# Kernel optimization log

Hardware: AMD Instinct MI355X
Metric: run time of the kernel (lower is better)

The kernel has to match this reference:

```python
import jax, jax.numpy as jnp
import numpy as np

D = 128  # input_dim

def setup_inputs() -> dict:
    key = jax.random.key(0)
    ks = jax.random.split(key, 9)
    B, Lq, Lkv = 4, 4096, 4096
    s = 1.0 / np.sqrt(D)
    return {
        "x1": jax.random.normal(ks[0], (B, Lq, D), dtype=jnp.float32),
        "x2": jax.random.normal(ks[1], (B, Lkv, D), dtype=jnp.float32),
        "x3": jax.random.normal(ks[2], (B, Lkv, D), dtype=jnp.float32),
        "Wq": jax.random.normal(ks[3], (D, D), dtype=jnp.float32) * s,
        "bq": jax.random.normal(ks[4], (D,), dtype=jnp.float32) * s,
        "Wk": jax.random.normal(ks[5], (D, D), dtype=jnp.float32) * s,
        "bk": jax.random.normal(ks[6], (D,), dtype=jnp.float32) * s,
        "Wv": jax.random.normal(ks[7], (D, D), dtype=jnp.float32) * s,
        "bv": jax.random.normal(ks[8], (D,), dtype=jnp.float32) * s,
    }

def reference(x1, x2, x3, Wq, bq, Wk, bk, Wv, bv):
    # torch Linear: y = x @ W.T + b
    q = jnp.einsum('bld,ed->ble', x1, Wq) + bq  # [B,Lq,D]
    k = jnp.einsum('bld,ed->ble', x2, Wk) + bk  # [B,Lkv,D]
    v = jnp.einsum('bld,ed->ble', x3, Wv) + bv  # [B,Lkv,D]
    scores = jnp.einsum('bqd,bkd->bqk', q, k) / jnp.sqrt(jnp.float32(x1.shape[-1]))
    attn = jax.nn.softmax(scores, axis=2)
    return jnp.einsum('bqk,bkd->bqd', attn, v)
```

## Files before the change

kernel.cpp:

```cpp
#include <hip/hip_runtime.h>
#include <hip/hip_bf16.h>

typedef __attribute__((ext_vector_type(8))) short short8;
typedef __attribute__((ext_vector_type(4))) float v4f;

__device__ __forceinline__ unsigned short f2bf(float f) {
    union { float f; unsigned u; } c; c.f = f;
    unsigned r = c.u + 0x7FFFu + ((c.u >> 16) & 1u);
    return (unsigned short)(r >> 16);
}
__device__ __forceinline__ unsigned pack2(float a, float b) {
    return (unsigned)f2bf(a) | ((unsigned)f2bf(b) << 16);
}
__device__ __forceinline__ float bf2f(unsigned short h) {
    union { unsigned u; float f; } c; c.u = ((unsigned)h) << 16;
    return c.f;
}

__device__ __forceinline__ void g2l16(const unsigned short* g, unsigned short* l) {
    __builtin_amdgcn_global_load_lds(
        (const __attribute__((address_space(1))) unsigned int*)g,
        (__attribute__((address_space(3))) unsigned int*)l,
        16, 0, 0);
}

__global__ __launch_bounds__(512) void proj_kernel(
    const float* __restrict__ x1, const float* __restrict__ x2, const float* __restrict__ x3,
    const float* __restrict__ Wq, const float* __restrict__ bq,
    const float* __restrict__ Wk, const float* __restrict__ bk,
    const float* __restrict__ Wv, const float* __restrict__ bv,
    unsigned short* __restrict__ qb, unsigned short* __restrict__ kb,
    unsigned short* __restrict__ vb, float qscale)
{
    __shared__ __attribute__((aligned(16))) unsigned short Xs[16384];
    __shared__ __attribute__((aligned(16))) unsigned short Ws[16384];

    int tid = threadIdx.x;
    int wave = tid >> 6, lane = tid & 63;
    int lmod = lane & 15, ldiv = lane >> 4;
    int p = blockIdx.x % 3;
    int row0 = (blockIdx.x / 3) * 128;

    const float* X = p == 0 ? x1 : p == 1 ? x2 : x3;
    const float* W = p == 0 ? Wq : p == 1 ? Wk : Wv;
    const float* bias = p == 0 ? bq : p == 1 ? bk : bv;
    float scale = p == 0 ? qscale : 1.0f;

#pragma unroll
    for (int i = 0; i < 8; i++) {
        int c = tid + i * 512;
        int row = c >> 5, d0 = (c & 31) * 4;
        v4f f = *(const v4f*)(X + (size_t)(row0 + row) * 128 + d0);
        int off = ((row >> 4) * 16 + (d0 >> 5) * 4 + ((d0 >> 3) & 3)) * 128 + (row & 15) * 8 + (d0 & 7);
        *(uint2*)&Xs[off] = make_uint2(pack2(f[0], f[1]), pack2(f[2], f[3]));
        v4f g = *(const v4f*)(W + (size_t)row * 128 + d0);
        *(uint2*)&Ws[off] = make_uint2(pack2(g[0], g[1]), pack2(g[2], g[3]));
    }
    __syncthreads();

    short8 af[4];
#pragma unroll
    for (int kc = 0; kc < 4; kc++)
        af[kc] = *(const short8*)&Xs[wave * 2048 + (kc * 4 + ldiv) * 128 + lmod * 8];

#pragma unroll
    for (int ct = 0; ct < 8; ct++) {
        v4f acc = {0.f, 0.f, 0.f, 0.f};
#pragma unroll
        for (int kc = 0; kc < 4; kc++) {
            short8 bf = *(const short8*)&Ws[ct * 2048 + (kc * 4 + ldiv) * 128 + lmod * 8];
            acc = __builtin_amdgcn_mfma_f32_16x16x32_bf16(af[kc], bf, acc, 0, 0, 0);
        }
        int e = ct * 16 + lmod;
        float bv_ = bias[e];
#pragma unroll
        for (int r = 0; r < 4; r++) {
            int orow = row0 + wave * 16 + ldiv * 4 + r;
            unsigned short h = f2bf((acc[r] + bv_) * scale);
            if (p == 0) {
                qb[(size_t)orow * 128 + e] = h;
            } else if (p == 1) {
                int b = orow >> 12, key = orow & 4095, kk = key & 31;
                kb[b * 524288 + (key >> 5) * 4096 + (kk & 1) * 2048
                   + ((e >> 5) * 4 + ((e >> 3) & 3)) * 128 + (kk >> 1) * 8 + (e & 7)] = h;
            } else {
                int b = orow >> 12, key = orow & 4095;
                vb[b * 524288 + (key >> 5) * 4096
                   + ((e >> 4) * 4 + ((key >> 3) & 3)) * 128 + (e & 15) * 8 + (key & 7)] = h;
            }
        }
    }
}

__global__ __launch_bounds__(256, 2) void attn_kernel(
    const unsigned short* __restrict__ Qb,
    const unsigned short* __restrict__ Kb,
    const unsigned short* __restrict__ Vb,
    unsigned short* __restrict__ Opart,
    float* __restrict__ Lbuf)
{
    __shared__ __attribute__((aligned(16))) unsigned short Kt[2][4096];
    __shared__ __attribute__((aligned(16))) unsigned short Vt[2][4096];
    __shared__ __attribute__((aligned(16))) unsigned short Ps[4][1280];

    int tid = threadIdx.x;
    int wave = tid >> 6, lane = tid & 63;
    int lmod = lane & 15, ldiv = lane >> 4;
    int split = blockIdx.x & 3;
    int qidx = blockIdx.x >> 2;
    int b = qidx >> 5;
    int q0 = (qidx & 31) * 128 + wave * 32;

    short8 qfrag[2][4];
#pragma unroll
    for (int set = 0; set < 2; set++) {
        const unsigned short* qptr = Qb + (size_t)(b * 4096 + q0 + set * 16 + lmod) * 128;
#pragma unroll
        for (int kc = 0; kc < 4; kc++)
            qfrag[set][kc] = *(const short8*)(qptr + kc * 32 + ldiv * 8);
    }

    v4f oacc[2][8];
#pragma unroll
    for (int set = 0; set < 2; set++)
#pragma unroll
        for (int dt = 0; dt < 8; dt++) oacc[set][dt] = (v4f){0.f, 0.f, 0.f, 0.f};
    float lsum[2][4] = {{0.f, 0.f, 0.f, 0.f}, {0.f, 0.f, 0.f, 0.f}};

    const unsigned short* kbase = Kb + b * 524288 + split * 131072;
    const unsigned short* vbase = Vb + b * 524288 + split * 131072;

#pragma unroll
    for (int i = 0; i < 2; i++) {
        g2l16(kbase + wave * 1024 + i * 512 + lane * 8, &Kt[0][wave * 1024 + i * 512]);
        g2l16(vbase + wave * 1024 + i * 512 + lane * 8, &Vt[0][wave * 1024 + i * 512]);
    }
    __syncthreads();

    for (int t = 0; t < 32; t++) {
        int cur = t & 1;
        if (t < 31) {
            const unsigned short* kg = kbase + (t + 1) * 4096;
            const unsigned short* vg = vbase + (t + 1) * 4096;
#pragma unroll
            for (int i = 0; i < 2; i++) {
                g2l16(kg + wave * 1024 + i * 512 + lane * 8, &Kt[cur ^ 1][wave * 1024 + i * 512]);
                g2l16(vg + wave * 1024 + i * 512 + lane * 8, &Vt[cur ^ 1][wave * 1024 + i * 512]);
            }
        }

        v4f sacc[2][2];
#pragma unroll
        for (int set = 0; set < 2; set++)
#pragma unroll
            for (int s = 0; s < 2; s++) sacc[set][s] = (v4f){0.f, 0.f, 0.f, 0.f};
#pragma unroll
        for (int kc = 0; kc < 4; kc++) {
            short8 kf0 = *(const short8*)&Kt[cur][(kc * 4 + ldiv) * 128 + lmod * 8];
            short8 kf1 = *(const short8*)&Kt[cur][2048 + (kc * 4 + ldiv) * 128 + lmod * 8];
            sacc[0][0] = __builtin_amdgcn_mfma_f32_16x16x32_bf16(qfrag[0][kc], kf0, sacc[0][0], 0, 0, 0);
            sacc[0][1] = __builtin_amdgcn_mfma_f32_16x16x32_bf16(qfrag[0][kc], kf1, sacc[0][1], 0, 0, 0);
            sacc[1][0] = __builtin_amdgcn_mfma_f32_16x16x32_bf16(qfrag[1][kc], kf0, sacc[1][0], 0, 0, 0);
            sacc[1][1] = __builtin_amdgcn_mfma_f32_16x16x32_bf16(qfrag[1][kc], kf1, sacc[1][1], 0, 0, 0);
        }

#pragma unroll
        for (int set = 0; set < 2; set++)
#pragma unroll
            for (int r = 0; r < 4; r++) {
                float p0 = __builtin_amdgcn_exp2f(sacc[set][0][r]);
                float p1 = __builtin_amdgcn_exp2f(sacc[set][1][r]);
                lsum[set][r] += p0 + p1;
                *(unsigned*)&Ps[wave][(set * 16 + 4 * ldiv + r) * 40 + lmod * 2] = pack2(p0, p1);
            }
        asm volatile("s_waitcnt lgkmcnt(0)" ::: "memory");

        short8 pf0 = *(const short8*)&Ps[wave][lmod * 40 + ldiv * 8];
        short8 pf1 = *(const short8*)&Ps[wave][(16 + lmod) * 40 + ldiv * 8];
#pragma unroll
        for (int dt = 0; dt < 8; dt++) {
            short8 vf = *(const short8*)&Vt[cur][(dt * 4 + ldiv) * 128 + lmod * 8];
            oacc[0][dt] = __builtin_amdgcn_mfma_f32_16x16x32_bf16(pf0, vf, oacc[0][dt], 0, 0, 0);
            oacc[1][dt] = __builtin_amdgcn_mfma_f32_16x16x32_bf16(pf1, vf, oacc[1][dt], 0, 0, 0);
        }
        __syncthreads();
    }

#pragma unroll
    for (int set = 0; set < 2; set++)
#pragma unroll
        for (int r = 0; r < 4; r++) {
            float lv = lsum[set][r];
            lv += __shfl_xor(lv, 1);
            lv += __shfl_xor(lv, 2);
            lv += __shfl_xor(lv, 4);
            lv += __shfl_xor(lv, 8);
            int gq = b * 4096 + q0 + set * 16 + 4 * ldiv + r;
            if (lmod == 0) Lbuf[split * 16384 + gq] = lv;
            unsigned short* obase = Opart + (size_t)(split * 16384 + gq) * 128;
#pragma unroll
            for (int dt = 0; dt < 8; dt++)
                obase[dt * 16 + lmod] = f2bf(oacc[set][dt][r]);
        }
}

__global__ __launch_bounds__(256) void merge_kernel(
    const unsigned short* __restrict__ Opart,
    const float* __restrict__ Lbuf,
    float* __restrict__ Out)
{
    int t = blockIdx.x * 256 + threadIdx.x;
#pragma unroll
    for (int it = 0; it < 4; it++) {
        int base = (t + it * 65536) * 8;
        int q = base >> 7;
        float inv = 1.0f / (Lbuf[q] + Lbuf[16384 + q] + Lbuf[32768 + q] + Lbuf[49152 + q]);
        float acc[8] = {0.f, 0.f, 0.f, 0.f, 0.f, 0.f, 0.f, 0.f};
#pragma unroll
        for (int s = 0; s < 4; s++) {
            short8 o = *(const short8*)(Opart + (size_t)s * 2097152 + base);
#pragma unroll
            for (int j = 0; j < 8; j++) acc[j] += bf2f((unsigned short)o[j]);
        }
        v4f lo = {acc[0] * inv, acc[1] * inv, acc[2] * inv, acc[3] * inv};
        v4f hi = {acc[4] * inv, acc[5] * inv, acc[6] * inv, acc[7] * inv};
        *(v4f*)(Out + base) = lo;
        *(v4f*)(Out + base + 4) = hi;
    }
}

extern "C" void kernel_launch(void* const* d_in, const int* in_sizes, int n_in,
                              void* d_out, int out_size, void* d_ws, size_t ws_size,
                              hipStream_t stream) {
    const float* x1 = (const float*)d_in[0];
    const float* x2 = (const float*)d_in[1];
    const float* x3 = (const float*)d_in[2];
    const float* Wq = (const float*)d_in[3];
    const float* bq = (const float*)d_in[4];
    const float* Wk = (const float*)d_in[5];
    const float* bk = (const float*)d_in[6];
    const float* Wv = (const float*)d_in[7];
    const float* bv = (const float*)d_in[8];
    float* out = (float*)d_out;

    unsigned short* qb = (unsigned short*)d_ws;
    unsigned short* kb = qb + (size_t)2097152;
    unsigned short* vb = kb + (size_t)2097152;
    unsigned short* op = vb + (size_t)2097152;
    float* lb = (float*)(op + (size_t)8388608);

    const float qscale = 1.4426950408889634f / 11.313708498984761f;

    proj_kernel<<<384, 512, 0, stream>>>(x1, x2, x3, Wq, bq, Wk, bk, Wv, bv,
                                         qb, kb, vb, qscale);
    attn_kernel<<<512, 256, 0, stream>>>(qb, kb, vb, op, lb);
    merge_kernel<<<256, 256, 0, stream>>>(op, lb, out);
}
```

Baseline: 140.8 us.

## Split KV within block across wave pairs, halve global splits, stage projection stores

The attention kernel now gives each block 64 queries and two KV groups: wave pairs share Q tiles while processing different 32-key halves of a 64-key tile. The two partial results are reduced in-block through shared memory, so the global split count drops from 4 to 2 and the merge kernel reads half as many partials. The projection kernel stages its bf16 outputs in shared memory and writes them out with coalesced 16-byte stores instead of scattered 2-byte stores. The attention block uses more shared memory (about 74KB), which may limit occupancy, and it adds an in-block reduction step.

```diff
diff --git a/kernel.cpp b/kernel.cpp
--- a/kernel.cpp
+++ b/kernel.cpp
@@ -3,6 +3,7 @@
 
 typedef __attribute__((ext_vector_type(8))) short short8;
 typedef __attribute__((ext_vector_type(4))) float v4f;
+typedef __attribute__((ext_vector_type(4))) unsigned int uint4v;
 
 __device__ __forceinline__ unsigned short f2bf(float f) {
     union { float f; unsigned u; } c; c.f = f;
@@ -32,8 +33,10 @@
     unsigned short* __restrict__ qb, unsigned short* __restrict__ kb,
     unsigned short* __restrict__ vb, float qscale)
 {
-    __shared__ __attribute__((aligned(16))) unsigned short Xs[16384];
-    __shared__ __attribute__((aligned(16))) unsigned short Ws[16384];
+    __shared__ __attribute__((aligned(16))) unsigned short Smem[32768];
+    unsigned short* Xs = Smem;
+    unsigned short* Ws = Smem + 16384;
+    unsigned short* Os = Smem;
 
     int tid = threadIdx.x;
     int wave = tid >> 6, lane = tid & 63;
@@ -62,6 +65,7 @@
 #pragma unroll
     for (int kc = 0; kc < 4; kc++)
         af[kc] = *(const short8*)&Xs[wave * 2048 + (kc * 4 + ldiv) * 128 + lmod * 8];
+    __syncthreads();
 
 #pragma unroll
     for (int ct = 0; ct < 8; ct++) {
@@ -75,20 +79,36 @@
         float bv_ = bias[e];
 #pragma unroll
         for (int r = 0; r < 4; r++) {
-            int orow = row0 + wave * 16 + ldiv * 4 + r;
+            int lrow = wave * 16 + ldiv * 4 + r;
             unsigned short h = f2bf((acc[r] + bv_) * scale);
+            int off;
             if (p == 0) {
-                qb[(size_t)orow * 128 + e] = h;
+                off = lrow * 128 + e;
             } else if (p == 1) {
-                int b = orow >> 12, key = orow & 4095, kk = key & 31;
-                kb[b * 524288 + (key >> 5) * 4096 + (kk & 1) * 2048
-                   + ((e >> 5) * 4 + ((e >> 3) & 3)) * 128 + (kk >> 1) * 8 + (e & 7)] = h;
+                int kk = lrow & 31, c = lrow >> 5;
+                off = c * 4096 + (kk & 1) * 2048
+                    + ((e >> 5) * 4 + ((e >> 3) & 3)) * 128 + (kk >> 1) * 8 + (e & 7);
             } else {
-                int b = orow >> 12, key = orow & 4095;
-                vb[b * 524288 + (key >> 5) * 4096
-                   + ((e >> 4) * 4 + ((key >> 3) & 3)) * 128 + (e & 15) * 8 + (key & 7)] = h;
-            }
-        }
+                int c = lrow >> 5;
+                off = c * 4096 + ((e >> 4) * 4 + ((lrow >> 3) & 3)) * 128 + (e & 15) * 8 + (lrow & 7);
+            }
+            Os[off] = h;
+        }
+    }
+    __syncthreads();
+
+    unsigned short* dst;
+    size_t gbase;
+    if (p == 0) { dst = qb; gbase = (size_t)row0 * 128; }
+    else {
+        int b = row0 >> 12, key0 = row0 & 4095;
+        gbase = (size_t)b * 524288 + (key0 >> 5) * 4096;
+        dst = (p == 1) ? kb : vb;
+    }
+#pragma unroll
+    for (int i = 0; i < 4; i++) {
+        int c = (tid + i * 512) * 8;
+        *(uint4v*)(dst + gbase + c) = *(const uint4v*)&Os[c];
     }
 }
 
@@ -99,17 +119,19 @@
     unsigned short* __restrict__ Opart,
     float* __restrict__ Lbuf)
 {
-    __shared__ __attribute__((aligned(16))) unsigned short Kt[2][4096];
-    __shared__ __attribute__((aligned(16))) unsigned short Vt[2][4096];
-    __shared__ __attribute__((aligned(16))) unsigned short Ps[4][1280];
+    __shared__ __attribute__((aligned(16))) unsigned short Smem[2 * 8192 + 2 * 8192 + 4 * 1280];
+    unsigned short* KtB = Smem;
+    unsigned short* VtB = Smem + 16384;
+    unsigned short* PsB = Smem + 32768;
 
     int tid = threadIdx.x;
     int wave = tid >> 6, lane = tid & 63;
     int lmod = lane & 15, ldiv = lane >> 4;
-    int split = blockIdx.x & 3;
-    int qidx = blockIdx.x >> 2;
-    int b = qidx >> 5;
-    int q0 = (qidx & 31) * 128 + wave * 32;
+    int qt = wave & 1, kg = wave >> 1;
+    int split = blockIdx.x & 1;
+    int rest = blockIdx.x >> 1;
+    int b = rest >> 6;
+    int q0 = (rest & 63) * 64 + qt * 32;
 
     short8 qfrag[2][4];
 #pragma unroll
@@ -127,25 +149,28 @@
         for (int dt = 0; dt < 8; dt++) oacc[set][dt] = (v4f){0.f, 0.f, 0.f, 0.f};
     float lsum[2][4] = {{0.f, 0.f, 0.f, 0.f}, {0.f, 0.f, 0.f, 0.f}};
 
-    const unsigned short* kbase = Kb + b * 524288 + split * 131072;
-    const unsigned short* vbase = Vb + b * 524288 + split * 131072;
-
-#pragma unroll
-    for (int i = 0; i < 2; i++) {
-        g2l16(kbase + wave * 1024 + i * 512 + lane * 8, &Kt[0][wave * 1024 + i * 512]);
-        g2l16(vbase + wave * 1024 + i * 512 + lane * 8, &Vt[0][wave * 1024 + i * 512]);
+    const unsigned short* kbase = Kb + (size_t)b * 524288 + split * 262144;
+    const unsigned short* vbase = Vb + (size_t)b * 524288 + split * 262144;
+
+#pragma unroll
+    for (int i = 0; i < 4; i++) {
+        g2l16(kbase + wave * 2048 + i * 512 + lane * 8, &KtB[wave * 2048 + i * 512]);
+        g2l16(vbase + wave * 2048 + i * 512 + lane * 8, &VtB[wave * 2048 + i * 512]);
     }
     __syncthreads();
 
     for (int t = 0; t < 32; t++) {
         int cur = t & 1;
+        unsigned short* Kt = KtB + cur * 8192 + kg * 4096;
+        unsigned short* Vt = VtB + cur * 8192 + kg * 4096;
         if (t < 31) {
-            const unsigned short* kg = kbase + (t + 1) * 4096;
-            const unsigned short* vg = vbase + (t + 1) * 4096;
-#pragma unroll
-            for (int i = 0; i < 2; i++) {
-                g2l16(kg + wave * 1024 + i * 512 + lane * 8, &Kt[cur ^ 1][wave * 1024 + i * 512]);
-                g2l16(vg + wave * 1024 + i * 512 + lane * 8, &Vt[cur ^ 1][wave * 1024 + i * 512]);
+            const unsigned short* kg_ = kbase + (t + 1) * 8192;
+            const unsigned short* vg_ = vbase + (t + 1) * 8192;
+            int nb = (cur ^ 1) * 8192;
+#pragma unroll
+            for (int i = 0; i < 4; i++) {
+                g2l16(kg_ + wave * 2048 + i * 512 + lane * 8, &KtB[nb + wave * 2048 + i * 512]);
+                g2l16(vg_ + wave * 2048 + i * 512 + lane * 8, &VtB[nb + wave * 2048 + i * 512]);
             }
         }
 
@@ -156,14 +181,15 @@
             for (int s = 0; s < 2; s++) sacc[set][s] = (v4f){0.f, 0.f, 0.f, 0.f};
 #pragma unroll
         for (int kc = 0; kc < 4; kc++) {
-            short8 kf0 = *(const short8*)&Kt[cur][(kc * 4 + ldiv) * 128 + lmod * 8];
-            short8 kf1 = *(const short8*)&Kt[cur][2048 + (kc * 4 + ldiv) * 128 + lmod * 8];
+            short8 kf0 = *(const short8*)&Kt[(kc * 4 + ldiv) * 128 + lmod * 8];
+            short8 kf1 = *(const short8*)&Kt[2048 + (kc * 4 + ldiv) * 128 + lmod * 8];
             sacc[0][0] = __builtin_amdgcn_mfma_f32_16x16x32_bf16(qfrag[0][kc], kf0, sacc[0][0], 0, 0, 0);
             sacc[0][1] = __builtin_amdgcn_mfma_f32_16x16x32_bf16(qfrag[0][kc], kf1, sacc[0][1], 0, 0, 0);
             sacc[1][0] = __builtin_amdgcn_mfma_f32_16x16x32_bf16(qfrag[1][kc], kf0, sacc[1][0], 0, 0, 0);
             sacc[1][1] = __builtin_amdgcn_mfma_f32_16x16x32_bf16(qfrag[1][kc], kf1, sacc[1][1], 0, 0, 0);
         }
 
+        unsigned short* Ps = PsB + wave * 1280;
 #pragma unroll
         for (int set = 0; set < 2; set++)
 #pragma unroll
@@ -171,21 +197,22 @@
                 float p0 = __builtin_amdgcn_exp2f(sacc[set][0][r]);
                 float p1 = __builtin_amdgcn_exp2f(sacc[set][1][r]);
                 lsum[set][r] += p0 + p1;
-                *(unsigned*)&Ps[wave][(set * 16 + 4 * ldiv + r) * 40 + lmod * 2] = pack2(p0, p1);
+                *(unsigned*)&Ps[(set * 16 + 4 * ldiv + r) * 40 + lmod * 2] = pack2(p0, p1);
             }
         asm volatile("s_waitcnt lgkmcnt(0)" ::: "memory");
 
-        short8 pf0 = *(const short8*)&Ps[wave][lmod * 40 + ldiv * 8];
-        short8 pf1 = *(const short8*)&Ps[wave][(16 + lmod) * 40 + ldiv * 8];
+        short8 pf0 = *(const short8*)&Ps[lmod * 40 + ldiv * 8];
+        short8 pf1 = *(const short8*)&Ps[(16 + lmod) * 40 + ldiv * 8];
 #pragma unroll
         for (int dt = 0; dt < 8; dt++) {
-            short8 vf = *(const short8*)&Vt[cur][(dt * 4 + ldiv) * 128 + lmod * 8];
+            short8 vf = *(const short8*)&Vt[(dt * 4 + ldiv) * 128 + lmod * 8];
             oacc[0][dt] = __builtin_amdgcn_mfma_f32_16x16x32_bf16(pf0, vf, oacc[0][dt], 0, 0, 0);
             oacc[1][dt] = __builtin_amdgcn_mfma_f32_16x16x32_bf16(pf1, vf, oacc[1][dt], 0, 0, 0);
         }
         __syncthreads();
     }
 
+    float lred[2][4];
 #pragma unroll
     for (int set = 0; set < 2; set++)
 #pragma unroll
@@ -195,13 +222,38 @@
             lv += __shfl_xor(lv, 2);
             lv += __shfl_xor(lv, 4);
             lv += __shfl_xor(lv, 8);
-            int gq = b * 4096 + q0 + set * 16 + 4 * ldiv + r;
-            if (lmod == 0) Lbuf[split * 16384 + gq] = lv;
-            unsigned short* obase = Opart + (size_t)(split * 16384 + gq) * 128;
-#pragma unroll
-            for (int dt = 0; dt < 8; dt++)
-                obase[dt * 16 + lmod] = f2bf(oacc[set][dt][r]);
-        }
+            lred[set][r] = lv;
+        }
+
+    float* Obuf = (float*)Smem;
+    float* Lb2  = (float*)PsB;
+    if (kg == 1) {
+#pragma unroll
+        for (int set = 0; set < 2; set++)
+#pragma unroll
+            for (int r = 0; r < 4; r++) {
+                int row = qt * 32 + set * 16 + 4 * ldiv + r;
+#pragma unroll
+                for (int dt = 0; dt < 8; dt++)
+                    Obuf[row * 130 + dt * 16 + lmod] = oacc[set][dt][r];
+                if (lmod == 0) Lb2[row] = lred[set][r];
+            }
+    }
+    __syncthreads();
+    if (kg == 0) {
+#pragma unroll
+        for (int set = 0; set < 2; set++)
+#pragma unroll
+            for (int r = 0; r < 4; r++) {
+                int row = qt * 32 + set * 16 + 4 * ldiv + r;
+                int gq = b * 4096 + q0 + set * 16 + 4 * ldiv + r;
+                if (lmod == 0) Lbuf[split * 16384 + gq] = lred[set][r] + Lb2[row];
+                unsigned short* obase = Opart + (size_t)(split * 16384 + gq) * 128;
+#pragma unroll
+                for (int dt = 0; dt < 8; dt++)
+                    obase[dt * 16 + lmod] = f2bf(oacc[set][dt][r] + Obuf[row * 130 + dt * 16 + lmod]);
+            }
+    }
 }
 
 __global__ __launch_bounds__(256) void merge_kernel(
@@ -214,18 +266,15 @@
     for (int it = 0; it < 4; it++) {
         int base = (t + it * 65536) * 8;
         int q = base >> 7;
-        float inv = 1.0f / (Lbuf[q] + Lbuf[16384 + q] + Lbuf[32768 + q] + Lbuf[49152 + q]);
-        float acc[8] = {0.f, 0.f, 0.f, 0.f, 0.f, 0.f, 0.f, 0.f};
-#pragma unroll
-        for (int s = 0; s < 4; s++) {
-            short8 o = *(const short8*)(Opart + (size_t)s * 2097152 + base);
-#pragma unroll
-            for (int j = 0; j < 8; j++) acc[j] += bf2f((unsigned short)o[j]);
-        }
-        v4f lo = {acc[0] * inv, acc[1] * inv, acc[2] * inv, acc[3] * inv};
-        v4f hi = {acc[4] * inv, acc[5] * inv, acc[6] * inv, acc[7] * inv};
-        *(v4f*)(Out + base) = lo;
-        *(v4f*)(Out + base + 4) = hi;
+        float inv = 1.0f / (Lbuf[q] + Lbuf[16384 + q]);
+        short8 o0 = *(const short8*)(Opart + base);
+        short8 o1 = *(const short8*)(Opart + 2097152 + base);
+        float acc[8];
+#pragma unroll
+        for (int j = 0; j < 8; j++)
+            acc[j] = (bf2f((unsigned short)o0[j]) + bf2f((unsigned short)o1[j])) * inv;
+        *(v4f*)(Out + base) = (v4f){acc[0], acc[1], acc[2], acc[3]};
+        *(v4f*)(Out + base + 4) = (v4f){acc[4], acc[5], acc[6], acc[7]};
     }
 }
 
@@ -247,7 +296,7 @@
     unsigned short* kb = qb + (size_t)2097152;
     unsigned short* vb = kb + (size_t)2097152;
     unsigned short* op = vb + (size_t)2097152;
-    float* lb = (float*)(op + (size_t)8388608);
+    float* lb = (float*)(op + (size_t)4194304);
 
     const float qscale = 1.4426950408889634f / 11.313708498984761f;
 
```

Result: no change. 142.7 us (+1.4%).

## Fuse projection, attention and merge into one persistent kernel with grid barriers

Applied to the files above, without the earlier changes.

Replaces the three launches with a single 512-block persistent kernel. It runs the projection, the split-KV attention and the merge as phases separated by a software grid barrier built on an atomic counter. The projection phase now uses 32-row tiles and stages outputs in LDS so K/V/Q are written with coalesced 16-byte stores instead of scattered 2-byte stores. The aim is to cut launch gaps and tail effects. The cost is that it relies on all 512 blocks being co-resident (2 per CU) and adds barrier spin overhead. The projection also reloads and converts the full weight matrix for each 32-row tile.

```diff
diff --git a/kernel.cpp b/kernel.cpp
--- a/kernel.cpp
+++ b/kernel.cpp
@@ -3,6 +3,9 @@
 
 typedef __attribute__((ext_vector_type(8))) short short8;
 typedef __attribute__((ext_vector_type(4))) float v4f;
+typedef __attribute__((ext_vector_type(4))) unsigned int uint4v;
+
+__device__ unsigned g_ctr;
 
 __device__ __forceinline__ unsigned short f2bf(float f) {
     union { float f; unsigned u; } c; c.f = f;
@@ -16,7 +19,6 @@
     union { unsigned u; float f; } c; c.u = ((unsigned)h) << 16;
     return c.f;
 }
-
 __device__ __forceinline__ void g2l16(const unsigned short* g, unsigned short* l) {
     __builtin_amdgcn_global_load_lds(
         (const __attribute__((address_space(1))) unsigned int*)g,
@@ -24,208 +26,249 @@
         16, 0, 0);
 }
 
-__global__ __launch_bounds__(512) void proj_kernel(
+__device__ __forceinline__ void grid_barrier() {
+    __syncthreads();
+    if (threadIdx.x == 0) {
+        __threadfence();
+        unsigned old = __hip_atomic_fetch_add(&g_ctr, 1u, __ATOMIC_ACQ_REL,
+                                              __HIP_MEMORY_SCOPE_AGENT);
+        unsigned target = old - (old & 511u) + 512u;
+        while (__hip_atomic_load(&g_ctr, __ATOMIC_ACQUIRE,
+                                 __HIP_MEMORY_SCOPE_AGENT) < target)
+            __builtin_amdgcn_s_sleep(8);
+        __threadfence();
+    }
+    __syncthreads();
+}
+
+__global__ __launch_bounds__(256, 2) void fused_kernel(
     const float* __restrict__ x1, const float* __restrict__ x2, const float* __restrict__ x3,
     const float* __restrict__ Wq, const float* __restrict__ bq,
     const float* __restrict__ Wk, const float* __restrict__ bk,
     const float* __restrict__ Wv, const float* __restrict__ bv,
     unsigned short* __restrict__ qb, unsigned short* __restrict__ kb,
-    unsigned short* __restrict__ vb, float qscale)
+    unsigned short* __restrict__ vb, unsigned short* __restrict__ Opart,
+    float* __restrict__ Lbuf, float* __restrict__ Out, float qscale)
 {
-    __shared__ __attribute__((aligned(16))) unsigned short Xs[16384];
-    __shared__ __attribute__((aligned(16))) unsigned short Ws[16384];
+    __shared__ __attribute__((aligned(16))) unsigned short Smem[24576];
 
     int tid = threadIdx.x;
     int wave = tid >> 6, lane = tid & 63;
     int lmod = lane & 15, ldiv = lane >> 4;
-    int p = blockIdx.x % 3;
-    int row0 = (blockIdx.x / 3) * 128;
-
-    const float* X = p == 0 ? x1 : p == 1 ? x2 : x3;
-    const float* W = p == 0 ? Wq : p == 1 ? Wk : Wv;
-    const float* bias = p == 0 ? bq : p == 1 ? bk : bv;
-    float scale = p == 0 ? qscale : 1.0f;
-
-#pragma unroll
-    for (int i = 0; i < 8; i++) {
-        int c = tid + i * 512;
-        int row = c >> 5, d0 = (c & 31) * 4;
-        v4f f = *(const v4f*)(X + (size_t)(row0 + row) * 128 + d0);
-        int off = ((row >> 4) * 16 + (d0 >> 5) * 4 + ((d0 >> 3) & 3)) * 128 + (row & 15) * 8 + (d0 & 7);
-        *(uint2*)&Xs[off] = make_uint2(pack2(f[0], f[1]), pack2(f[2], f[3]));
-        v4f g = *(const v4f*)(W + (size_t)row * 128 + d0);
-        *(uint2*)&Ws[off] = make_uint2(pack2(g[0], g[1]), pack2(g[2], g[3]));
-    }
-    __syncthreads();
-
-    short8 af[4];
-#pragma unroll
-    for (int kc = 0; kc < 4; kc++)
-        af[kc] = *(const short8*)&Xs[wave * 2048 + (kc * 4 + ldiv) * 128 + lmod * 8];
-
-#pragma unroll
-    for (int ct = 0; ct < 8; ct++) {
-        v4f acc = {0.f, 0.f, 0.f, 0.f};
-#pragma unroll
-        for (int kc = 0; kc < 4; kc++) {
-            short8 bf = *(const short8*)&Ws[ct * 2048 + (kc * 4 + ldiv) * 128 + lmod * 8];
-            acc = __builtin_amdgcn_mfma_f32_16x16x32_bf16(af[kc], bf, acc, 0, 0, 0);
-        }
-        int e = ct * 16 + lmod;
-        float bv_ = bias[e];
-#pragma unroll
-        for (int r = 0; r < 4; r++) {
-            int orow = row0 + wave * 16 + ldiv * 4 + r;
-            unsigned short h = f2bf((acc[r] + bv_) * scale);
-            if (p == 0) {
-                qb[(size_t)orow * 128 + e] = h;
-            } else if (p == 1) {
-                int b = orow >> 12, key = orow & 4095, kk = key & 31;
-                kb[b * 524288 + (key >> 5) * 4096 + (kk & 1) * 2048
-                   + ((e >> 5) * 4 + ((e >> 3) & 3)) * 128 + (kk >> 1) * 8 + (e & 7)] = h;
-            } else {
-                int b = orow >> 12, key = orow & 4095;
-                vb[b * 524288 + (key >> 5) * 4096
-                   + ((e >> 4) * 4 + ((key >> 3) & 3)) * 128 + (e & 15) * 8 + (key & 7)] = h;
-            }
-        }
-    }
-}
-
-__global__ __launch_bounds__(256, 2) void attn_kernel(
-    const unsigned short* __restrict__ Qb,
-    const unsigned short* __restrict__ Kb,
-    const unsigned short* __restrict__ Vb,
-    unsigned short* __restrict__ Opart,
-    float* __restrict__ Lbuf)
-{
-    __shared__ __attribute__((aligned(16))) unsigned short Kt[2][4096];
-    __shared__ __attribute__((aligned(16))) unsigned short Vt[2][4096];
-    __shared__ __attribute__((aligned(16))) unsigned short Ps[4][1280];
-
-    int tid = threadIdx.x;
-    int wave = tid >> 6, lane = tid & 63;
-    int lmod = lane & 15, ldiv = lane >> 4;
-    int split = blockIdx.x & 3;
-    int qidx = blockIdx.x >> 2;
-    int b = qidx >> 5;
-    int q0 = (qidx & 31) * 128 + wave * 32;
-
-    short8 qfrag[2][4];
-#pragma unroll
-    for (int set = 0; set < 2; set++) {
-        const unsigned short* qptr = Qb + (size_t)(b * 4096 + q0 + set * 16 + lmod) * 128;
-#pragma unroll
-        for (int kc = 0; kc < 4; kc++)
-            qfrag[set][kc] = *(const short8*)(qptr + kc * 32 + ldiv * 8);
-    }
-
-    v4f oacc[2][8];
-#pragma unroll
-    for (int set = 0; set < 2; set++)
-#pragma unroll
-        for (int dt = 0; dt < 8; dt++) oacc[set][dt] = (v4f){0.f, 0.f, 0.f, 0.f};
-    float lsum[2][4] = {{0.f, 0.f, 0.f, 0.f}, {0.f, 0.f, 0.f, 0.f}};
-
-    const unsigned short* kbase = Kb + b * 524288 + split * 131072;
-    const unsigned short* vbase = Vb + b * 524288 + split * 131072;
-
-#pragma unroll
-    for (int i = 0; i < 2; i++) {
-        g2l16(kbase + wave * 1024 + i * 512 + lane * 8, &Kt[0][wave * 1024 + i * 512]);
-        g2l16(vbase + wave * 1024 + i * 512 + lane * 8, &Vt[0][wave * 1024 + i * 512]);
-    }
-    __syncthreads();
-
-    for (int t = 0; t < 32; t++) {
-        int cur = t & 1;
-        if (t < 31) {
-            const unsigned short* kg = kbase + (t + 1) * 4096;
-            const unsigned short* vg = vbase + (t + 1) * 4096;
+
+    {
+        unsigned short* Xs = Smem;
+        unsigned short* Ws = Smem + 4096;
+        unsigned short* Os = Smem;
+
+        for (int u = blockIdx.x; u < 1536; u += 512) {
+            __syncthreads();
+            int p = u >> 9;
+            int row0 = (u & 511) * 32;
+            const float* X = p == 0 ? x1 : p == 1 ? x2 : x3;
+            const float* W = p == 0 ? Wq : p == 1 ? Wk : Wv;
+            const float* bias = p == 0 ? bq : p == 1 ? bk : bv;
+            float scale = p == 0 ? qscale : 1.0f;
+
+#pragma unroll
+            for (int i = 0; i < 4; i++) {
+                int c = tid + i * 256;
+                int row = c >> 5, d0 = (c & 31) * 4;
+                v4f f = *(const v4f*)(X + (size_t)(row0 + row) * 128 + d0);
+                int off = ((row >> 4) * 16 + (d0 >> 5) * 4 + ((d0 >> 3) & 3)) * 128
+                        + (row & 15) * 8 + (d0 & 7);
+                *(uint2*)&Xs[off] = make_uint2(pack2(f[0], f[1]), pack2(f[2], f[3]));
+            }
+#pragma unroll
+            for (int i = 0; i < 16; i++) {
+                int c = tid + i * 256;
+                int e = c >> 5, d0 = (c & 31) * 4;
+                v4f g = *(const v4f*)(W + (size_t)e * 128 + d0);
+                int off = ((e >> 4) * 16 + (d0 >> 5) * 4 + ((d0 >> 3) & 3)) * 128
+                        + (e & 15) * 8 + (d0 & 7);
+                *(uint2*)&Ws[off] = make_uint2(pack2(g[0], g[1]), pack2(g[2], g[3]));
+            }
+            __syncthreads();
+
+            int grp = wave & 1, ctb = (wave >> 1) * 4;
+            short8 af[4];
+#pragma unroll
+            for (int kc = 0; kc < 4; kc++)
+                af[kc] = *(const short8*)&Xs[(grp * 16 + kc * 4 + ldiv) * 128 + lmod * 8];
+            __syncthreads();
+
+#pragma unroll
+            for (int c2 = 0; c2 < 4; c2++) {
+                int ct = ctb + c2;
+                v4f acc = {0.f, 0.f, 0.f, 0.f};
+#pragma unroll
+                for (int kc = 0; kc < 4; kc++) {
+                    short8 bf = *(const short8*)&Ws[(ct * 16 + kc * 4 + ldiv) * 128 + lmod * 8];
+                    acc = __builtin_amdgcn_mfma_f32_16x16x32_bf16(af[kc], bf, acc, 0, 0, 0);
+                }
+                int e = ct * 16 + lmod;
+                float bv_ = bias[e];
+#pragma unroll
+                for (int r = 0; r < 4; r++) {
+                    int lrow = grp * 16 + ldiv * 4 + r;
+                    unsigned short h = f2bf((acc[r] + bv_) * scale);
+                    int off;
+                    if (p == 0) {
+                        off = lrow * 128 + e;
+                    } else if (p == 1) {
+                        off = (lrow & 1) * 2048 + ((e >> 5) * 4 + ((e >> 3) & 3)) * 128
+                            + (lrow >> 1) * 8 + (e & 7);
+                    } else {
+                        off = ((e >> 4) * 4 + ((lrow >> 3) & 3)) * 128
+                            + (e & 15) * 8 + (lrow & 7);
+                    }
+                    Os[off] = h;
+                }
+            }
+            __syncthreads();
+
+            unsigned short* dst;
+            size_t gbase;
+            if (p == 0) { dst = qb; gbase = (size_t)row0 * 128; }
+            else {
+                int b = row0 >> 12, key0 = row0 & 4095;
+                gbase = (size_t)b * 524288 + (key0 >> 5) * 4096;
+                dst = (p == 1) ? kb : vb;
+            }
 #pragma unroll
             for (int i = 0; i < 2; i++) {
-                g2l16(kg + wave * 1024 + i * 512 + lane * 8, &Kt[cur ^ 1][wave * 1024 + i * 512]);
-                g2l16(vg + wave * 1024 + i * 512 + lane * 8, &Vt[cur ^ 1][wave * 1024 + i * 512]);
-            }
-        }
-
-        v4f sacc[2][2];
+                int c = (tid + i * 256) * 8;
+                *(uint4v*)(dst + gbase + c) = *(const uint4v*)&Os[c];
+            }
+        }
+    }
+    grid_barrier();
+
+    {
+        unsigned short* KtB = Smem;
+        unsigned short* VtB = Smem + 8192;
+        unsigned short* PsB = Smem + 16384;
+
+        int split = blockIdx.x & 3;
+        int qidx = blockIdx.x >> 2;
+        int b = qidx >> 5;
+        int q0 = (qidx & 31) * 128 + wave * 32;
+
+        short8 qfrag[2][4];
+#pragma unroll
+        for (int set = 0; set < 2; set++) {
+            const unsigned short* qptr = qb + (size_t)(b * 4096 + q0 + set * 16 + lmod) * 128;
+#pragma unroll
+            for (int kc = 0; kc < 4; kc++)
+                qfrag[set][kc] = *(const short8*)(qptr + kc * 32 + ldiv * 8);
+        }
+
+        v4f oacc[2][8];
 #pragma unroll
         for (int set = 0; set < 2; set++)
 #pragma unroll
-            for (int s = 0; s < 2; s++) sacc[set][s] = (v4f){0.f, 0.f, 0.f, 0.f};
-#pragma unroll
-        for (int kc = 0; kc < 4; kc++) {
-            short8 kf0 = *(const short8*)&Kt[cur][(kc * 4 + ldiv) * 128 + lmod * 8];
-            short8 kf1 = *(const short8*)&Kt[cur][2048 + (kc * 4 + ldiv) * 128 + lmod * 8];
-            sacc[0][0] = __builtin_amdgcn_mfma_f32_16x16x32_bf16(qfrag[0][kc], kf0, sacc[0][0], 0, 0, 0);
-            sacc[0][1] = __builtin_amdgcn_mfma_f32_16x16x32_bf16(qfrag[0][kc], kf1, sacc[0][1], 0, 0, 0);
-            sacc[1][0] = __builtin_amdgcn_mfma_f32_16x16x32_bf16(qfrag[1][kc], kf0, sacc[1][0], 0, 0, 0);
-            sacc[1][1] = __builtin_amdgcn_mfma_f32_16x16x32_bf16(qfrag[1][kc], kf1, sacc[1][1], 0, 0, 0);
+            for (int dt = 0; dt < 8; dt++) oacc[set][dt] = (v4f){0.f, 0.f, 0.f, 0.f};
+        float lsum[2][4] = {{0.f, 0.f, 0.f, 0.f}, {0.f, 0.f, 0.f, 0.f}};
+
+        const unsigned short* kbase = kb + (size_t)b * 524288 + split * 131072;
+        const unsigned short* vbase = vb + (size_t)b * 524288 + split * 131072;
+
+#pragma unroll
+        for (int i = 0; i < 2; i++) {
+            g2l16(kbase + wave * 1024 + i * 512 + lane * 8, KtB + wave * 1024 + i * 512);
+            g2l16(vbase + wave * 1024 + i * 512 + lane * 8, VtB + wave * 1024 + i * 512);
+        }
+        __syncthreads();
+
+        for (int t = 0; t < 32; t++) {
+            int cur = t & 1;
+            unsigned short* Kt = KtB + cur * 4096;
+            unsigned short* Vt = VtB + cur * 4096;
+            if (t < 31) {
+                const unsigned short* kg = kbase + (t + 1) * 4096;
+                const unsigned short* vg = vbase + (t + 1) * 4096;
+                int nb = (cur ^ 1) * 4096;
+#pragma unroll
+                for (int i = 0; i < 2; i++) {
+                    g2l16(kg + wave * 1024 + i * 512 + lane * 8, KtB + nb + wave * 1024 + i * 512);
+                    g2l16(vg + wave * 1024 + i * 512 + lane * 8, VtB + nb + wave * 1024 + i * 512);
+                }
+            }
+
+            v4f sacc[2][2];
+#pragma unroll
+            for (int set = 0; set < 2; set++)
+#pragma unroll
+                for (int s = 0; s < 2; s++) sacc[set][s] = (v4f){0.f, 0.f, 0.f, 0.f};
+#pragma unroll
+            for (int kc = 0; kc < 4; kc++) {
+                short8 kf0 = *(const short8*)&Kt[(kc * 4 + ldiv) * 128 + lmod * 8];
+                short8 kf1 = *(const short8*)&Kt[2048 + (kc * 4 + ldiv) * 128 + lmod * 8];
+                sacc[0][0] = __builtin_amdgcn_mfma_f32_16x16x32_bf16(qfrag[0][kc], kf0, sacc[0][0], 0, 0, 0);
+                sacc[0][1] = __builtin_amdgcn_mfma_f32_16x16x32_bf16(qfrag[0][kc], kf1, sacc[0][1], 0, 0, 0);
+                sacc[1][0] = __builtin_amdgcn_mfma_f32_16x16x32_bf16(qfrag[1][kc], kf0, sacc[1][0], 0, 0, 0);
+                sacc[1][1] = __builtin_amdgcn_mfma_f32_16x16x32_bf16(qfrag[1][kc], kf1, sacc[1][1], 0, 0, 0);
+            }
+
+            unsigned short* Ps = PsB + wave * 1280;
+#pragma unroll
+            for (int set = 0; set < 2; set++)
+#pragma unroll
+                for (int r = 0; r < 4; r++) {
+                    float p0 = __builtin_amdgcn_exp2f(sacc[set][0][r]);
+                    float p1 = __builtin_amdgcn_exp2f(sacc[set][1][r]);
+                    lsum[set][r] += p0 + p1;
+                    *(unsigned*)&Ps[(set * 16 + 4 * ldiv + r) * 40 + lmod * 2] = pack2(p0, p1);
+                }
+            asm volatile("s_waitcnt lgkmcnt(0)" ::: "memory");
+
+            short8 pf0 = *(const short8*)&Ps[lmod * 40 + ldiv * 8];
+            short8 pf1 = *(const short8*)&Ps[(16 + lmod) * 40 + ldiv * 8];
+#pragma unroll
+            for (int dt = 0; dt < 8; dt++) {
+                short8 vf = *(const short8*)&Vt[(dt * 4 + ldiv) * 128 + lmod * 8];
+                oacc[0][dt] = __builtin_amdgcn_mfma_f32_16x16x32_bf16(pf0, vf, oacc[0][dt], 0, 0, 0);
+                oacc[1][dt] = __builtin_amdgcn_mfma_f32_16x16x32_bf16(pf1, vf, oacc[1][dt], 0, 0, 0);
+            }
+            __syncthreads();
         }
 
 #pragma unroll
         for (int set = 0; set < 2; set++)
 #pragma unroll
             for (int r = 0; r < 4; r++) {
-                float p0 = __builtin_amdgcn_exp2f(sacc[set][0][r]);
-                float p1 = __builtin_amdgcn_exp2f(sacc[set][1][r]);
-                lsum[set][r] += p0 + p1;
-                *(unsigned*)&Ps[wave][(set * 16 + 4 * ldiv + r) * 40 + lmod * 2] = pack2(p0, p1);
-            }
-        asm volatile("s_waitcnt lgkmcnt(0)" ::: "memory");
-
-        short8 pf0 = *(const short8*)&Ps[wave][lmod * 40 + ldiv * 8];
-        short8 pf1 = *(const short8*)&Ps[wave][(16 + lmod) * 40 + ldiv * 8];
-#pragma unroll
-        for (int dt = 0; dt < 8; dt++) {
-            short8 vf = *(const short8*)&Vt[cur][(dt * 4 + ldiv) * 128 + lmod * 8];
-            oacc[0][dt] = __builtin_amdgcn_mfma_f32_16x16x32_bf16(pf0, vf, oacc[0][dt], 0, 0, 0);
-            oacc[1][dt] = __builtin_amdgcn_mfma_f32_16x16x32_bf16(pf1, vf, oacc[1][dt], 0, 0, 0);
-        }
-        __syncthreads();
-    }
-
-#pragma unroll
-    for (int set = 0; set < 2; set++)
-#pragma unroll
-        for (int r = 0; r < 4; r++) {
-            float lv = lsum[set][r];
-            lv += __shfl_xor(lv, 1);
-            lv += __shfl_xor(lv, 2);
-            lv += __shfl_xor(lv, 4);
-            lv += __shfl_xor(lv, 8);
-            int gq = b * 4096 + q0 + set * 16 + 4 * ldiv + r;
-            if (lmod == 0) Lbuf[split * 16384 + gq] = lv;
-            unsigned short* obase = Opart + (size_t)(split * 16384 + gq) * 128;
-#pragma unroll
-            for (int dt = 0; dt < 8; dt++)
-                obase[dt * 16 + lmod] = f2bf(oacc[set][dt][r]);
-        }
-}
-
-__global__ __launch_bounds__(256) void merge_kernel(
-    const unsigned short* __restrict__ Opart,
-    const float* __restrict__ Lbuf,
-    float* __restrict__ Out)
-{
-    int t = blockIdx.x * 256 + threadIdx.x;
-#pragma unroll
-    for (int it = 0; it < 4; it++) {
-        int base = (t + it * 65536) * 8;
-        int q = base >> 7;
-        float inv = 1.0f / (Lbuf[q] + Lbuf[16384 + q] + Lbuf[32768 + q] + Lbuf[49152 + q]);
-        float acc[8] = {0.f, 0.f, 0.f, 0.f, 0.f, 0.f, 0.f, 0.f};
-#pragma unroll
-        for (int s = 0; s < 4; s++) {
-            short8 o = *(const short8*)(Opart + (size_t)s * 2097152 + base);
-#pragma unroll
-            for (int j = 0; j < 8; j++) acc[j] += bf2f((unsigned short)o[j]);
-        }
-        v4f lo = {acc[0] * inv, acc[1] * inv, acc[2] * inv, acc[3] * inv};
-        v4f hi = {acc[4] * inv, acc[5] * inv, acc[6] * inv, acc[7] * inv};
-        *(v4f*)(Out + base) = lo;
-        *(v4f*)(Out + base + 4) = hi;
+                float lv = lsum[set][r];
+                lv += __shfl_xor(lv, 1);
+                lv += __shfl_xor(lv, 2);
+                lv += __shfl_xor(lv, 4);
+                lv += __shfl_xor(lv, 8);
+                int gq = b * 4096 + q0 + set * 16 + 4 * ldiv + r;
+                if (lmod == 0) Lbuf[split * 16384 + gq] = lv;
+                unsigned short* obase = Opart + (size_t)(split * 16384 + gq) * 128;
+#pragma unroll
+                for (int dt = 0; dt < 8; dt++)
+                    obase[dt * 16 + lmod] = f2bf(oacc[set][dt][r]);
+            }
+    }
+    grid_barrier();
+
+    {
+        int t = blockIdx.x * 256 + tid;
+#pragma unroll
+        for (int j = 0; j < 2; j++) {
+            int base = t * 16 + j * 8;
+            int q = base >> 7;
+            float inv = 1.0f / (Lbuf[q] + Lbuf[16384 + q] + Lbuf[32768 + q] + Lbuf[49152 + q]);
+            float acc[8] = {0.f, 0.f, 0.f, 0.f, 0.f, 0.f, 0.f, 0.f};
+#pragma unroll
+            for (int s = 0; s < 4; s++) {
+                short8 o = *(const short8*)(Opart + (size_t)s * 2097152 + base);
+#pragma unroll
+                for (int k = 0; k < 8; k++) acc[k] += bf2f((unsigned short)o[k]);
+            }
+            *(v4f*)(Out + base) = (v4f){acc[0] * inv, acc[1] * inv, acc[2] * inv, acc[3] * inv};
+            *(v4f*)(Out + base + 4) = (v4f){acc[4] * inv, acc[5] * inv, acc[6] * inv, acc[7] * inv};
+        }
     }
 }
 
@@ -251,8 +294,6 @@
 
     const float qscale = 1.4426950408889634f / 11.313708498984761f;
 
-    proj_kernel<<<384, 512, 0, stream>>>(x1, x2, x3, Wq, bq, Wk, bk, Wv, bv,
-                                         qb, kb, vb, qscale);
-    attn_kernel<<<512, 256, 0, stream>>>(qb, kb, vb, op, lb);
-    merge_kernel<<<256, 256, 0, stream>>>(op, lb, out);
-}
+    fused_kernel<<<512, 256, 0, stream>>>(x1, x2, x3, Wq, bq, Wk, bk, Wv, bv,
+                                          qb, kb, vb, op, lb, out, qscale);
+}
```

Measured after the change: 290.3 us. 2.06x slower.
